# Performance work log

Hardware: AMD Instinct MI355X
Metric: run time of the kernel (lower is better)

Reference implementation:

```python
import jax, jax.numpy as jnp
import numpy as np

B, T, V, RNN, N_OBJ = 1024, 48, 2000, 64, 25

def _lstm_cell(x, h, c, W_ih, W_hh, b_ih, b_hh):
    # PyTorch LSTMCell: gate order i, f, g, o
    gates = x @ W_ih.T + h @ W_hh.T + b_ih + b_hh
    i, f, g, o = jnp.split(gates, 4, axis=-1)
    c2 = jax.nn.sigmoid(f) * c + jax.nn.sigmoid(i) * jnp.tanh(g)
    return jax.nn.sigmoid(o) * jnp.tanh(c2), c2

def _attend(memory, h2, w1, b1, w2, b2):
    # memory: [B, 25, 4], h2: [B, 25, RNN]
    x = jnp.concatenate([h2, memory], axis=2)            # [B, 25, RNN+4]
    s = (jax.nn.relu(x @ w1.T + b1) @ w2.T + b2)[..., 0]  # [B, 25]
    w = jax.nn.softmax(s, axis=1)
    return jnp.einsum('bn,bnd->bd', w, memory)            # [B, 4]

def setup_inputs() -> dict:
    key = jax.random.key(0)
    ks = jax.random.split(key, 32)
    f = lambda k, shape: jax.random.normal(k, shape, dtype=jnp.float32) * 0.05
    return dict(
        inst=jax.random.randint(ks[0], (B, T), 1, V + 1),
        prev_canvas=jax.random.uniform(ks[1], (B, N_OBJ, 4), dtype=jnp.float32),
        final_canvas=jax.random.uniform(ks[2], (B, N_OBJ, 4), dtype=jnp.float32),
        embed=f(ks[3], (V + 1, 64)),
        W_ih_att=f(ks[4], (4 * RNN, 128)), W_hh_att=f(ks[5], (4 * RNN, RNN)),
        b_ih_att=f(ks[6], (4 * RNN,)), b_hh_att=f(ks[7], (4 * RNN,)),
        W_ih_lang=f(ks[8], (4 * RNN, 2 * RNN)), W_hh_lang=f(ks[9], (4 * RNN, RNN)),
        b_ih_lang=f(ks[10], (4 * RNN,)), b_hh_lang=f(ks[11], (4 * RNN,)),
        fc_out_w=f(ks[12], (V + 1, RNN)), fc_out_b=f(ks[13], (V + 1,)),
        att1_w1=f(ks[14], (32, RNN + 4)), att1_b1=f(ks[15], (32,)),
        att1_w2=f(ks[16], (1, 32)), att1_b2=f(ks[17], (1,)),
        att2_w1=f(ks[18], (32, RNN + 4)), att2_b1=f(ks[19], (32,)),
        att2_w2=f(ks[20], (1, 32)), att2_b2=f(ks[21], (1,)),
        trans_w1=f(ks[22], (32, 8)), trans_b1=f(ks[23], (32,)),
        trans_w2=f(ks[24], (RNN, 32)), trans_b2=f(ks[25], (RNN,)),
    )

def reference(inst, prev_canvas, final_canvas, embed, W_ih_att, W_hh_att, b_ih_att, b_hh_att, W_ih_lang, W_hh_lang, b_ih_lang, b_hh_lang, fc_out_w, fc_out_b, att1_w1, att1_b1, att1_w2, att1_b2, att2_w1, att2_b1, att2_w2, att2_b2, trans_w1, trans_b1, trans_w2, trans_b2):
    # compute_diff_canvas
    mask = prev_canvas.sum(axis=2, keepdims=True) > 0
    diff_canvas = jnp.where(mask, -1.0, final_canvas)  # [B, 25, 4]
    batch = inst.shape[0]
    h0 = jnp.zeros((batch, RNN), dtype=jnp.float32)

    def step(carry, it):
        h_att, c_att, h_lang, c_lang = carry
        xt = embed[it]  # [B, 64]
        h_att, c_att = _lstm_cell(jnp.concatenate([h_lang, xt], axis=1), h_att, c_att, W_ih_att, W_hh_att, b_ih_att, b_hh_att)
        h2 = jnp.broadcast_to(h_att[:, None, :], (batch, N_OBJ, RNN))
        a1 = _attend(diff_canvas, h2, att1_w1, att1_b1, att1_w2, att1_b2)
        a2 = _attend(prev_canvas, h2, att2_w1, att2_b1, att2_w2, att2_b2)
        att = jnp.concatenate([a1, a2], axis=1)  # [B, 8]
        att = jax.nn.relu(att @ trans_w1.T + trans_b1) @ trans_w2.T + trans_b2  # [B, RNN]
        h_lang, c_lang = _lstm_cell(jnp.concatenate([att, h_att], axis=1), h_lang, c_lang, W_ih_lang, W_hh_lang, b_ih_lang, b_hh_lang)
        logp = jax.nn.log_softmax(h_lang @ fc_out_w.T + fc_out_b, axis=1)  # [B, V+1]
        return (h_att, c_att, h_lang, c_lang), logp

    xs = inst[:, :-1].T  # [T-1, B]; inst has no all-zero column so all steps run
    _, outs = jax.lax.scan(step, (h0, h0, h0, h0), xs)
    return jnp.transpose(outs, (1, 0, 2))  # [B, T-1, V+1]
```

## Files before the change

### kernel.cpp

```cpp
#include <hip/hip_runtime.h>

#define BATCH 1024
#define TT 48
#define NSTEP 47
#define VOC 2001
#define RNN 64
#define NOBJ 25
#define NROWS (BATCH*NSTEP)
#define NTILE 126
#define NPAD 2016

typedef _Float16 h2 __attribute__((ext_vector_type(2)));
typedef _Float16 h8 __attribute__((ext_vector_type(8)));
typedef short short8 __attribute__((ext_vector_type(8)));
typedef float f32x4 __attribute__((ext_vector_type(4)));

__device__ __forceinline__ float fdot2f(h2 a, h2 b, float c){
#if __has_builtin(__builtin_amdgcn_fdot2)
    return __builtin_amdgcn_fdot2(a, b, c, false);
#else
    return c + (float)a[0]*(float)b[0] + (float)a[1]*(float)b[1];
#endif
}

__device__ __forceinline__ float dot8(h8 w, h8 x, float acc){
    acc = fdot2f(__builtin_shufflevector(w,w,0,1), __builtin_shufflevector(x,x,0,1), acc);
    acc = fdot2f(__builtin_shufflevector(w,w,2,3), __builtin_shufflevector(x,x,2,3), acc);
    acc = fdot2f(__builtin_shufflevector(w,w,4,5), __builtin_shufflevector(x,x,4,5), acc);
    acc = fdot2f(__builtin_shufflevector(w,w,6,7), __builtin_shufflevector(x,x,6,7), acc);
    return acc;
}

__device__ __forceinline__ float sigf(float x){ return 1.f/(1.f+__expf(-x)); }
__device__ __forceinline__ float tanh_(float x){
    float e = __expf(2.f*fminf(x, 15.f));
    return (e-1.f)/(e+1.f);
}
__device__ __forceinline__ unsigned short bf16r(float f){
    unsigned u = __float_as_uint(f);
    return (unsigned short)((u + 0x7FFFu + ((u>>16)&1u)) >> 16);
}

__device__ __forceinline__ void block_sync_lds(){
    asm volatile("s_waitcnt lgkmcnt(0)" ::: "memory");
    __builtin_amdgcn_s_barrier();
    asm volatile("" ::: "memory");
}


__global__ void k_pre(const float* __restrict__ prev, const float* __restrict__ fin,
                      const float* __restrict__ a1w1, const float* __restrict__ a1b1,
                      const float* __restrict__ a2w1, const float* __restrict__ a2b1,
                      float* __restrict__ diff, float* __restrict__ pre1, float* __restrict__ pre2){
    int idx = blockIdx.x*256 + threadIdx.x;
    if (idx >= BATCH*NOBJ) return;
    float p0 = prev[idx*4+0], p1 = prev[idx*4+1], p2 = prev[idx*4+2], p3 = prev[idx*4+3];
    bool masked = (p0+p1+p2+p3) > 0.f;
    float d0 = masked ? -1.f : fin[idx*4+0];
    float d1 = masked ? -1.f : fin[idx*4+1];
    float d2 = masked ? -1.f : fin[idx*4+2];
    float d3 = masked ? -1.f : fin[idx*4+3];
    diff[idx*4+0]=d0; diff[idx*4+1]=d1; diff[idx*4+2]=d2; diff[idx*4+3]=d3;
    for (int j=0;j<32;++j){
        const float* w1 = a1w1 + j*68 + 64;
        const float* w2 = a2w1 + j*68 + 64;
        pre1[idx*32+j] = a1b1[j] + d0*w1[0] + d1*w1[1] + d2*w1[2] + d3*w1[3];
        pre2[idx*32+j] = a2b1[j] + p0*w2[0] + p1*w2[1] + p2*w2[2] + p3*w2[3];
    }
}

__global__ void k_embw(const float* __restrict__ embed, const float* __restrict__ Wia,
                       const float* __restrict__ bia, const float* __restrict__ bha,
                       float* __restrict__ embW){
    int v = blockIdx.x, g = threadIdx.x;
    __shared__ float er[64];
    if (g < 64) er[g] = embed[v*64+g];
    __syncthreads();
    float acc = bia[g] + bha[g];
    const float* wr = Wia + g*128 + 64;
    #pragma unroll 8
    for (int k=0;k<64;++k) acc += er[k]*wr[k];
    embW[v*256+g] = acc;
}

__global__ void k_packrow(const float* __restrict__ src, _Float16* __restrict__ dst,
                          int srcK, int koff, int K, int total){
    int idx = blockIdx.x*256 + threadIdx.x;
    if (idx >= total) return;
    int k = idx % K, g = idx / K;
    dst[idx] = (_Float16)src[g*srcK + koff + k];
}

__global__ void k_weff(const float* __restrict__ Wil, const float* __restrict__ tw2,
                       const float* __restrict__ tb2, const float* __restrict__ bil,
                       const float* __restrict__ bhl, _Float16* __restrict__ Weff,
                       float* __restrict__ biasL2){
    __shared__ float t2[64*32];
    int g = threadIdx.x;
    for (int i=g;i<2048;i+=256) t2[i] = tw2[i];
    __syncthreads();
    float accs[32];
    #pragma unroll
    for (int m=0;m<32;++m) accs[m]=0.f;
    float bf = bil[g] + bhl[g];
    for (int d=0;d<64;++d){
        float w = Wil[g*128 + d];
        bf += w * tb2[d];
        #pragma unroll
        for (int m=0;m<32;++m) accs[m] += w * t2[d*32+m];
    }
    #pragma unroll
    for (int m=0;m<32;++m) Weff[g*32+m] = (_Float16)accs[m];
    biasL2[g] = bf;
}

__global__ void k_fcbpad(const float* __restrict__ fcb_in, float* __restrict__ fcb){
    int i = blockIdx.x*256 + threadIdx.x;
    if (i >= NPAD) return;
    fcb[i] = (i < VOC) ? fcb_in[i] : -1e30f;
}

__global__ void k_fragb(const float* __restrict__ fcw, unsigned short* __restrict__ fragB){
    int idx = blockIdx.x*256 + threadIdx.x;
    int lane = idx & 63, kh = (idx>>6)&1, tile = idx>>7;
    int n = tile*16 + (lane & 15);
    int k = kh*32 + (lane >> 4)*8;
    unsigned short* d = fragB + (size_t)((tile*2+kh)*64 + lane)*8;
    #pragma unroll
    for (int i=0;i<8;++i)
        d[i] = (n < VOC) ? bf16r(fcw[n*64 + k + i]) : (unsigned short)0;
}

__global__ __launch_bounds__(256, 2) void k_recur(
    const int* __restrict__ inst, const float* __restrict__ embW,
    const float* __restrict__ diff, const float* __restrict__ prev,
    const float* __restrict__ pre1, const float* __restrict__ pre2,
    const _Float16* __restrict__ attLp, const _Float16* __restrict__ attHp,
    const _Float16* __restrict__ wLhap, const _Float16* __restrict__ wLhlp,
    const _Float16* __restrict__ Weffp, const float* __restrict__ biasL2,
    const _Float16* __restrict__ w1fp,
    const float* __restrict__ a1w2, const float* __restrict__ a1b2,
    const float* __restrict__ a2w2, const float* __restrict__ a2b2,
    const float* __restrict__ tw1, const float* __restrict__ tb1,
    unsigned short* __restrict__ h_hist)
{
    const int tid = threadIdx.x;
    const int rb0 = blockIdx.x*2;

    __shared__ float gbuf[2][256];
    __shared__ __align__(16) _Float16 hl16[2][64];
    __shared__ __align__(16) _Float16 ha16[2][64];
    __shared__ __align__(16) _Float16 u16v[2][32];
    __shared__ float hpart[2][64];
    __shared__ float sbuf[2][2][32];
    __shared__ float att8s[2][8];
    __shared__ __align__(16) float preS[2][2][25][36];
    __shared__ float memS[2][200];
    __shared__ __align__(16) _Float16 w1fS[64*72];
    __shared__ float tw1T[256];
    __shared__ float w2S[2][32];
    __shared__ float b2S[2];
    __shared__ int   tokS[2][NSTEP];

    for (int i=tid;i<2*NSTEP;i+=256){ int r=i/NSTEP, s=i-r*NSTEP; tokS[r][s]=inst[(rb0+r)*TT+s]; }
    for (int i=tid;i<3200;i+=256){
        int r = i/1600, rem = i - r*1600, h = rem/800, rem2 = rem - h*800, n = rem2>>5, k = rem2&31;
        preS[r][h][n][k] = (h ? pre2 : pre1)[(size_t)((rb0+r)*NOBJ+n)*32 + k];
    }
    for (int i=tid;i<400;i+=256){
        int r = i/200, rem = i - r*200;
        memS[r][rem] = (rem<100 ? diff : prev)[(size_t)(rb0+r)*100 + (rem%100)];
    }
    for (int i=tid;i<4096;i+=256){
        int rw = i>>6, k = i&63;
        w1fS[rw*72+k] = w1fp[i];
    }
    { int m = tid&31, k = tid>>5; tw1T[k*32+m] = tw1[m*8+k]; }
    if (tid<64) w2S[tid>>5][tid&31] = (tid<32 ? a1w2 : a2w2)[tid&31];
    if (tid<2)  b2S[tid] = tid ? a2b2[0] : a1b2[0];
    for (int i=tid;i<128;i+=256){ hl16[i>>6][i&63]=(_Float16)0.f; ha16[i>>6][i&63]=(_Float16)0.f; }

    h8 wAL[8], wAH[8], wLHa[8], wLHl[8], wEf[4];
    {
        const h8* p0 = (const h8*)(attLp + (size_t)tid*64);
        const h8* p1 = (const h8*)(attHp + (size_t)tid*64);
        const h8* p2 = (const h8*)(wLhap + (size_t)tid*64);
        const h8* p3 = (const h8*)(wLhlp + (size_t)tid*64);
        const h8* p4 = (const h8*)(Weffp + (size_t)tid*32);
        #pragma unroll
        for (int k=0;k<8;++k){ wAL[k]=p0[k]; wAH[k]=p1[k]; wLHa[k]=p2[k]; wLHl[k]=p3[k]; }
        #pragma unroll
        for (int k=0;k<4;++k) wEf[k]=p4[k];
    }
    const float biasv = biasL2[tid];
    const float tb1v  = ((tid&63) < 32) ? tb1[tid&63] : 0.f;
    float c_att = 0.f, c_lang = 0.f;
    __syncthreads();

    const int wave = tid>>6, lane = tid&63;

    const h8* xh0 = (const h8*)&hl16[0][0];
    const h8* xh1 = (const h8*)&hl16[1][0];
    const h8* xa0 = (const h8*)&ha16[0][0];
    const h8* xa1 = (const h8*)&ha16[1][0];
    const h8* xu0 = (const h8*)&u16v[0][0];
    const h8* xu1 = (const h8*)&u16v[1][0];

    float ew0 = embW[(size_t)tokS[0][0]*256 + tid];
    float ew1 = embW[(size_t)tokS[1][0]*256 + tid];

    #pragma unroll 1
    for (int t=0;t<NSTEP;++t){
        float a0 = ew0, a1 = ew1, p0 = biasv, p1 = biasv;
        {
            int tn = (t+1 < NSTEP) ? t+1 : NSTEP-1;
            ew0 = embW[(size_t)tokS[0][tn]*256 + tid];
            ew1 = embW[(size_t)tokS[1][tn]*256 + tid];
        }
        #pragma unroll
        for (int k=0;k<8;++k){
            h8 h0 = xh0[k], h1 = xh1[k];
            a0 = dot8(wAL[k],  h0, a0);  a1 = dot8(wAL[k],  h1, a1);
            p0 = dot8(wLHl[k], h0, p0);  p1 = dot8(wLHl[k], h1, p1);
        }
        #pragma unroll
        for (int k=0;k<8;++k){
            h8 v0 = xa0[k], v1 = xa1[k];
            a0 = dot8(wAH[k], v0, a0);   a1 = dot8(wAH[k], v1, a1);
        }
        gbuf[0][tid] = a0; gbuf[1][tid] = a1;
        block_sync_lds();

        if (wave < 2){
            const int r = wave;
            float gi = gbuf[r][lane], gf = gbuf[r][64+lane];
            float gg = gbuf[r][128+lane], go = gbuf[r][192+lane];
            float i_=sigf(gi), f_=sigf(gf), g_=tanh_(gg), o_=sigf(go);
            c_att = f_*c_att + i_*g_;
            ha16[r][lane] = (_Float16)(o_*tanh_(c_att));
            {
                const h8* xa = (const h8*)&ha16[r][0];
                const h8* wr = (const h8*)&w1fS[lane*72];
                float hp = 0.f;
                #pragma unroll
                for (int k=0;k<8;++k) hp = dot8(wr[k], xa[k], hp);
                hpart[r][lane] = hp;
            }
            {
                int half = lane>>5, n = lane&31;
                if (n < NOBJ){
                    const float4* pp = (const float4*)&preS[r][half][n][0];
                    const float*  hp = &hpart[r][half*32];
                    const float*  w2 = &w2S[half][0];
                    float a = b2S[half];
                    #pragma unroll
                    for (int i=0;i<8;++i){
                        float4 pv = pp[i];
                        a += fmaxf(hp[4*i+0]+pv.x,0.f)*w2[4*i+0]
                           + fmaxf(hp[4*i+1]+pv.y,0.f)*w2[4*i+1]
                           + fmaxf(hp[4*i+2]+pv.z,0.f)*w2[4*i+2]
                           + fmaxf(hp[4*i+3]+pv.w,0.f)*w2[4*i+3];
                    }
                    sbuf[r][half][n] = a;
                }
            }
            if (lane < 8){
                int half = lane>>2, d = lane&3;
                const float* ss  = &sbuf[r][half][0];
                const float* mem = &memS[r][half*100];
                float m = -1e30f;
                for (int n=0;n<NOBJ;++n) m = fmaxf(m, ss[n]);
                float s=0.f, a=0.f;
                for (int n=0;n<NOBJ;++n){ float e=__expf(ss[n]-m); s+=e; a+=e*mem[n*4+d]; }
                att8s[r][lane] = a/s;
            }
            if (lane < 32){
                float u = tb1v;
                #pragma unroll
                for (int i=0;i<8;++i) u += att8s[r][i]*tw1T[i*32+lane];
                u16v[r][lane] = (_Float16)fmaxf(u, 0.f);
            }
        }
        block_sync_lds();

        #pragma unroll
        for (int k=0;k<4;++k){
            h8 u0 = xu0[k], u1 = xu1[k];
            p0 = dot8(wEf[k], u0, p0);   p1 = dot8(wEf[k], u1, p1);
        }
        #pragma unroll
        for (int k=0;k<8;++k){
            h8 v0 = xa0[k], v1 = xa1[k];
            p0 = dot8(wLHa[k], v0, p0);  p1 = dot8(wLHa[k], v1, p1);
        }
        gbuf[0][tid] = p0; gbuf[1][tid] = p1;
        block_sync_lds();

        if (wave < 2){
            const int r = wave;
            float gi = gbuf[r][lane], gf = gbuf[r][64+lane];
            float gg = gbuf[r][128+lane], go = gbuf[r][192+lane];
            float i_=sigf(gi), f_=sigf(gf), g_=tanh_(gg), o_=sigf(go);
            c_lang = f_*c_lang + i_*g_;
            float hL = o_*tanh_(c_lang);
            hl16[r][lane] = (_Float16)hL;
            h_hist[((size_t)(rb0+r)*NSTEP + t)*64 + lane] = bf16r(hL);
        }
        block_sync_lds();
    }
}


__global__ __launch_bounds__(256) void k_fc(const unsigned short* __restrict__ h_hist,
                                            const unsigned short* __restrict__ fragB,
                                            const float* __restrict__ fcb,
                                            float* __restrict__ out)
{
    const int tid = threadIdx.x;
    const int w = tid >> 6, lane = tid & 63;
    const int q = lane >> 4, l16 = lane & 15;
    const int rowbase = blockIdx.x*16;

    const short8 a0 = *(const short8*)(h_hist + (size_t)(rowbase + l16)*64 + q*8);
    const short8 a1 = *(const short8*)(h_hist + (size_t)(rowbase + l16)*64 + 32 + q*8);

    float m[4], s[4];
    #pragma unroll
    for (int i=0;i<4;++i){ m[i] = -INFINITY; s[i] = 0.f; }

    for (int tile = w; tile < NTILE; tile += 4){
        const short8 b0 = *(const short8*)(fragB + (size_t)((tile*2+0)*64 + lane)*8);
        const short8 b1 = *(const short8*)(fragB + (size_t)((tile*2+1)*64 + lane)*8);
        f32x4 acc = {0.f,0.f,0.f,0.f};
        acc = __builtin_amdgcn_mfma_f32_16x16x32_bf16(a0, b0, acc, 0, 0, 0);
        acc = __builtin_amdgcn_mfma_f32_16x16x32_bf16(a1, b1, acc, 0, 0, 0);
        float bias = fcb[tile*16 + l16];
        #pragma unroll
        for (int i=0;i<4;++i){
            float v = acc[i] + bias;
            float nm = fmaxf(m[i], v);
            s[i] = s[i]*__expf(m[i]-nm) + __expf(v-nm);
            m[i] = nm;
        }
    }
    #pragma unroll
    for (int i=0;i<4;++i){
        #pragma unroll
        for (int off=1; off<16; off<<=1){
            float om = __shfl_xor(m[i], off, 64);
            float os = __shfl_xor(s[i], off, 64);
            float nm = fmaxf(m[i], om);
            s[i] = s[i]*__expf(m[i]-nm) + os*__expf(om-nm);
            m[i] = nm;
        }
    }
    __shared__ float lm[4][16], ls[4][16], fm[16], fl[16];
    if (l16 == 0){
        #pragma unroll
        for (int i=0;i<4;++i){ lm[w][q*4+i] = m[i]; ls[w][q*4+i] = s[i]; }
    }
    __syncthreads();
    if (tid < 16){
        float M = -INFINITY, S = 0.f;
        #pragma unroll
        for (int ww=0;ww<4;++ww){
            float om = lm[ww][tid], os = ls[ww][tid];
            float nm = fmaxf(M, om);
            S = S*__expf(M-nm) + os*__expf(om-nm);
            M = nm;
        }
        fm[tid] = M; fl[tid] = __logf(S);
    }
    __syncthreads();
    float Mr[4], Lr[4];
    #pragma unroll
    for (int i=0;i<4;++i){ Mr[i] = fm[q*4+i]; Lr[i] = fl[q*4+i]; }

    for (int tile = w; tile < NTILE; tile += 4){
        const short8 b0 = *(const short8*)(fragB + (size_t)((tile*2+0)*64 + lane)*8);
        const short8 b1 = *(const short8*)(fragB + (size_t)((tile*2+1)*64 + lane)*8);
        f32x4 acc = {0.f,0.f,0.f,0.f};
        acc = __builtin_amdgcn_mfma_f32_16x16x32_bf16(a0, b0, acc, 0, 0, 0);
        acc = __builtin_amdgcn_mfma_f32_16x16x32_bf16(a1, b1, acc, 0, 0, 0);
        int col = tile*16 + l16;
        if (col < VOC){
            float bias = fcb[col];
            #pragma unroll
            for (int i=0;i<4;++i)
                out[(size_t)(rowbase + q*4 + i)*VOC + col] = acc[i] + bias - Mr[i] - Lr[i];
        }
    }
}


extern "C" void kernel_launch(void* const* d_in, const int* in_sizes, int n_in,
                              void* d_out, int out_size, void* d_ws, size_t ws_size,
                              hipStream_t stream)
{
    const int*   inst  = (const int*)  d_in[0];
    const float* prev  = (const float*)d_in[1];
    const float* fin   = (const float*)d_in[2];
    const float* embed = (const float*)d_in[3];
    const float* Wia   = (const float*)d_in[4];
    const float* Wha   = (const float*)d_in[5];
    const float* bia   = (const float*)d_in[6];
    const float* bha   = (const float*)d_in[7];
    const float* Wil   = (const float*)d_in[8];
    const float* Whl   = (const float*)d_in[9];
    const float* bil   = (const float*)d_in[10];
    const float* bhl   = (const float*)d_in[11];
    const float* fcw   = (const float*)d_in[12];
    const float* fcbi  = (const float*)d_in[13];
    const float* a1w1  = (const float*)d_in[14];
    const float* a1b1  = (const float*)d_in[15];
    const float* a1w2  = (const float*)d_in[16];
    const float* a1b2  = (const float*)d_in[17];
    const float* a2w1  = (const float*)d_in[18];
    const float* a2b1  = (const float*)d_in[19];
    const float* a2w2  = (const float*)d_in[20];
    const float* a2b2  = (const float*)d_in[21];
    const float* tw1   = (const float*)d_in[22];
    const float* tb1   = (const float*)d_in[23];
    const float* tw2   = (const float*)d_in[24];
    const float* tb2   = (const float*)d_in[25];
    float* out = (float*)d_out;

    char* wsb = (char*)d_ws; size_t off = 0;
    auto alloc = [&](size_t bytes)->char*{
        char* p = wsb + off; off = (off + bytes + 511) & ~(size_t)511; return p;
    };
    float*          embW  = (float*)alloc((size_t)VOC*256*4);
    float*          diff  = (float*)alloc((size_t)BATCH*NOBJ*4*4);
    float*          pre1  = (float*)alloc((size_t)BATCH*NOBJ*32*4);
    float*          pre2  = (float*)alloc((size_t)BATCH*NOBJ*32*4);
    _Float16*       attLp = (_Float16*)alloc((size_t)256*64*2);
    _Float16*       attHp = (_Float16*)alloc((size_t)256*64*2);
    _Float16*       wLhap = (_Float16*)alloc((size_t)256*64*2);
    _Float16*       wLhlp = (_Float16*)alloc((size_t)256*64*2);
    _Float16*       Weffp = (_Float16*)alloc((size_t)256*32*2);
    _Float16*       w1fp  = (_Float16*)alloc((size_t)64*64*2);
    float*          biasL2= (float*)alloc(256*4);
    float*          fcb   = (float*)alloc((size_t)NPAD*4);
    unsigned short* hhist = (unsigned short*)alloc((size_t)NROWS*64*2);
    unsigned short* fragB = (unsigned short*)alloc((size_t)NTILE*2*64*8*2);

    k_pre    <<<(BATCH*NOBJ+255)/256, 256, 0, stream>>>(prev, fin, a1w1, a1b1, a2w1, a2b1, diff, pre1, pre2);
    k_embw   <<<VOC, 256, 0, stream>>>(embed, Wia, bia, bha, embW);
    k_packrow<<<64, 256, 0, stream>>>(Wia, attLp, 128, 0,  64, 256*64);
    k_packrow<<<64, 256, 0, stream>>>(Wha, attHp,  64, 0,  64, 256*64);
    k_packrow<<<64, 256, 0, stream>>>(Wil, wLhap, 128, 64, 64, 256*64);
    k_packrow<<<64, 256, 0, stream>>>(Whl, wLhlp,  64, 0,  64, 256*64);
    k_packrow<<<8,  256, 0, stream>>>(a1w1, w1fp,       68, 0, 64, 32*64);
    k_packrow<<<8,  256, 0, stream>>>(a2w1, w1fp+32*64, 68, 0, 64, 32*64);
    k_weff   <<<1, 256, 0, stream>>>(Wil, tw2, tb2, bil, bhl, Weffp, biasL2);
    k_fcbpad <<<(NPAD+255)/256, 256, 0, stream>>>(fcbi, fcb);
    k_fragb  <<<63, 256, 0, stream>>>(fcw, fragB);

    k_recur<<<BATCH/2, 256, 0, stream>>>(inst, embW, diff, prev, pre1, pre2,
                                         attLp, attHp, wLhap, wLhlp, Weffp, biasL2, w1fp,
                                         a1w2, a1b2, a2w2, a2b2, tw1, tb1, hhist);

    k_fc<<<NROWS/16, 256, 0, stream>>>(hhist, fragB, fcb, out);
}
```

Measured before the change: 828.8 us.

## Split recurrent gate dot products across two thread halves and use shuffle-based softmax

The recurrent kernel now launches 512 threads per block; each half computes half of the K dimension for every gate row, and the partial sums are added when the gates are read from LDS. This halves the per-thread weight registers and the serial dot-product chain per step, which shortens the latency-bound recurrence. The attention softmax and weighted sum are also rewritten to use wave shuffles instead of a serial 25-iteration loop over LDS in 8 lanes. The cost is more threads per block, an extra LDS read per gate, and larger register and occupancy pressure under the new launch bounds.

```diff
diff --git a/kernel.cpp b/kernel.cpp
--- a/kernel.cpp
+++ b/kernel.cpp
@@ -131,7 +131,7 @@
         d[i] = (n < VOC) ? bf16r(fcw[n*64 + k + i]) : (unsigned short)0;
 }
 
-__global__ __launch_bounds__(256, 2) void k_recur(
+__global__ __launch_bounds__(512, 4) void k_recur(
     const int* __restrict__ inst, const float* __restrict__ embW,
     const float* __restrict__ diff, const float* __restrict__ prev,
     const float* __restrict__ pre1, const float* __restrict__ pre2,
@@ -144,97 +144,102 @@
     const float* __restrict__ tw1, const float* __restrict__ tb1,
     unsigned short* __restrict__ h_hist)
 {
-    const int tid = threadIdx.x;
-    const int rb0 = blockIdx.x*2;
-
-    __shared__ float gbuf[2][256];
+    const int tid  = threadIdx.x;
+    const int g    = tid & 255;
+    const int hh   = tid >> 8;
+    const int wave = tid >> 6, lane = tid & 63;
+    const int rb0  = blockIdx.x*2;
+
+    __shared__ float pbuf[2][2][256];
     __shared__ __align__(16) _Float16 hl16[2][64];
     __shared__ __align__(16) _Float16 ha16[2][64];
     __shared__ __align__(16) _Float16 u16v[2][32];
-    __shared__ float hpart[2][64];
-    __shared__ float sbuf[2][2][32];
-    __shared__ float att8s[2][8];
+    __shared__ __align__(16) float hpart[2][64];
     __shared__ __align__(16) float preS[2][2][25][36];
-    __shared__ float memS[2][200];
+    __shared__ __align__(16) float memS[2][200];
     __shared__ __align__(16) _Float16 w1fS[64*72];
     __shared__ float tw1T[256];
-    __shared__ float w2S[2][32];
+    __shared__ __align__(16) float w2S[2][32];
     __shared__ float b2S[2];
     __shared__ int   tokS[2][NSTEP];
 
-    for (int i=tid;i<2*NSTEP;i+=256){ int r=i/NSTEP, s=i-r*NSTEP; tokS[r][s]=inst[(rb0+r)*TT+s]; }
-    for (int i=tid;i<3200;i+=256){
+    for (int i=tid;i<2*NSTEP;i+=512){ int r=i/NSTEP, s=i-r*NSTEP; tokS[r][s]=inst[(rb0+r)*TT+s]; }
+    for (int i=tid;i<3200;i+=512){
         int r = i/1600, rem = i - r*1600, h = rem/800, rem2 = rem - h*800, n = rem2>>5, k = rem2&31;
         preS[r][h][n][k] = (h ? pre2 : pre1)[(size_t)((rb0+r)*NOBJ+n)*32 + k];
     }
-    for (int i=tid;i<400;i+=256){
+    for (int i=tid;i<400;i+=512){
         int r = i/200, rem = i - r*200;
         memS[r][rem] = (rem<100 ? diff : prev)[(size_t)(rb0+r)*100 + (rem%100)];
     }
-    for (int i=tid;i<4096;i+=256){
+    for (int i=tid;i<4096;i+=512){
         int rw = i>>6, k = i&63;
         w1fS[rw*72+k] = w1fp[i];
     }
-    { int m = tid&31, k = tid>>5; tw1T[k*32+m] = tw1[m*8+k]; }
+    if (tid<256){ int m = tid&31, k = tid>>5; tw1T[k*32+m] = tw1[m*8+k]; }
     if (tid<64) w2S[tid>>5][tid&31] = (tid<32 ? a1w2 : a2w2)[tid&31];
     if (tid<2)  b2S[tid] = tid ? a2b2[0] : a1b2[0];
-    for (int i=tid;i<128;i+=256){ hl16[i>>6][i&63]=(_Float16)0.f; ha16[i>>6][i&63]=(_Float16)0.f; }
-
-    h8 wAL[8], wAH[8], wLHa[8], wLHl[8], wEf[4];
+    if (tid<128){ hl16[tid>>6][tid&63]=(_Float16)0.f; ha16[tid>>6][tid&63]=(_Float16)0.f; }
+
+    h8 wAL[4], wAH[4], wLHa[4], wLHl[4], wEf[2];
     {
-        const h8* p0 = (const h8*)(attLp + (size_t)tid*64);
-        const h8* p1 = (const h8*)(attHp + (size_t)tid*64);
-        const h8* p2 = (const h8*)(wLhap + (size_t)tid*64);
-        const h8* p3 = (const h8*)(wLhlp + (size_t)tid*64);
-        const h8* p4 = (const h8*)(Weffp + (size_t)tid*32);
-        #pragma unroll
-        for (int k=0;k<8;++k){ wAL[k]=p0[k]; wAH[k]=p1[k]; wLHa[k]=p2[k]; wLHl[k]=p3[k]; }
-        #pragma unroll
-        for (int k=0;k<4;++k) wEf[k]=p4[k];
-    }
-    const float biasv = biasL2[tid];
-    const float tb1v  = ((tid&63) < 32) ? tb1[tid&63] : 0.f;
+        const h8* p0 = (const h8*)(attLp + (size_t)g*64 + hh*32);
+        const h8* p1 = (const h8*)(attHp + (size_t)g*64 + hh*32);
+        const h8* p2 = (const h8*)(wLhap + (size_t)g*64 + hh*32);
+        const h8* p3 = (const h8*)(wLhlp + (size_t)g*64 + hh*32);
+        const h8* p4 = (const h8*)(Weffp + (size_t)g*32 + hh*16);
+        #pragma unroll
+        for (int k=0;k<4;++k){ wAL[k]=p0[k]; wAH[k]=p1[k]; wLHa[k]=p2[k]; wLHl[k]=p3[k]; }
+        wEf[0]=p4[0]; wEf[1]=p4[1];
+    }
+    const float biasv = hh ? 0.f : biasL2[g];
+    const float tb1v  = (lane < 32) ? tb1[lane] : 0.f;
     float c_att = 0.f, c_lang = 0.f;
     __syncthreads();
 
-    const int wave = tid>>6, lane = tid&63;
-
-    const h8* xh0 = (const h8*)&hl16[0][0];
-    const h8* xh1 = (const h8*)&hl16[1][0];
-    const h8* xa0 = (const h8*)&ha16[0][0];
-    const h8* xa1 = (const h8*)&ha16[1][0];
-    const h8* xu0 = (const h8*)&u16v[0][0];
-    const h8* xu1 = (const h8*)&u16v[1][0];
-
-    float ew0 = embW[(size_t)tokS[0][0]*256 + tid];
-    float ew1 = embW[(size_t)tokS[1][0]*256 + tid];
+    const h8* xh0 = (const h8*)&hl16[0][hh*32];
+    const h8* xh1 = (const h8*)&hl16[1][hh*32];
+    const h8* xa0 = (const h8*)&ha16[0][hh*32];
+    const h8* xa1 = (const h8*)&ha16[1][hh*32];
+    const h8* xu0 = (const h8*)&u16v[0][hh*16];
+    const h8* xu1 = (const h8*)&u16v[1][hh*16];
+
+    float ew0 = 0.f, ew1 = 0.f;
+    if (hh == 0){
+        ew0 = embW[(size_t)tokS[0][0]*256 + g];
+        ew1 = embW[(size_t)tokS[1][0]*256 + g];
+    }
 
     #pragma unroll 1
     for (int t=0;t<NSTEP;++t){
-        float a0 = ew0, a1 = ew1, p0 = biasv, p1 = biasv;
-        {
+        float a0 = hh ? 0.f : ew0;
+        float a1 = hh ? 0.f : ew1;
+        float p0 = biasv, p1 = biasv;
+        if (hh == 0){
             int tn = (t+1 < NSTEP) ? t+1 : NSTEP-1;
-            ew0 = embW[(size_t)tokS[0][tn]*256 + tid];
-            ew1 = embW[(size_t)tokS[1][tn]*256 + tid];
-        }
-        #pragma unroll
-        for (int k=0;k<8;++k){
+            ew0 = embW[(size_t)tokS[0][tn]*256 + g];
+            ew1 = embW[(size_t)tokS[1][tn]*256 + g];
+        }
+        #pragma unroll
+        for (int k=0;k<4;++k){
             h8 h0 = xh0[k], h1 = xh1[k];
             a0 = dot8(wAL[k],  h0, a0);  a1 = dot8(wAL[k],  h1, a1);
             p0 = dot8(wLHl[k], h0, p0);  p1 = dot8(wLHl[k], h1, p1);
         }
         #pragma unroll
-        for (int k=0;k<8;++k){
+        for (int k=0;k<4;++k){
             h8 v0 = xa0[k], v1 = xa1[k];
             a0 = dot8(wAH[k], v0, a0);   a1 = dot8(wAH[k], v1, a1);
         }
-        gbuf[0][tid] = a0; gbuf[1][tid] = a1;
+        pbuf[hh][0][g] = a0; pbuf[hh][1][g] = a1;
         block_sync_lds();
 
         if (wave < 2){
             const int r = wave;
-            float gi = gbuf[r][lane], gf = gbuf[r][64+lane];
-            float gg = gbuf[r][128+lane], go = gbuf[r][192+lane];
+            float gi = pbuf[0][r][lane]     + pbuf[1][r][lane];
+            float gf = pbuf[0][r][64+lane]  + pbuf[1][r][64+lane];
+            float gg = pbuf[0][r][128+lane] + pbuf[1][r][128+lane];
+            float go = pbuf[0][r][192+lane] + pbuf[1][r][192+lane];
             float i_=sigf(gi), f_=sigf(gf), g_=tanh_(gg), o_=sigf(go);
             c_att = f_*c_att + i_*g_;
             ha16[r][lane] = (_Float16)(o_*tanh_(c_att));
@@ -246,60 +251,71 @@
                 for (int k=0;k<8;++k) hp = dot8(wr[k], xa[k], hp);
                 hpart[r][lane] = hp;
             }
+            const int half = lane>>5, n = lane&31;
+            float sc;
             {
-                int half = lane>>5, n = lane&31;
-                if (n < NOBJ){
-                    const float4* pp = (const float4*)&preS[r][half][n][0];
-                    const float*  hp = &hpart[r][half*32];
-                    const float*  w2 = &w2S[half][0];
-                    float a = b2S[half];
-                    #pragma unroll
-                    for (int i=0;i<8;++i){
-                        float4 pv = pp[i];
-                        a += fmaxf(hp[4*i+0]+pv.x,0.f)*w2[4*i+0]
-                           + fmaxf(hp[4*i+1]+pv.y,0.f)*w2[4*i+1]
-                           + fmaxf(hp[4*i+2]+pv.z,0.f)*w2[4*i+2]
-                           + fmaxf(hp[4*i+3]+pv.w,0.f)*w2[4*i+3];
-                    }
-                    sbuf[r][half][n] = a;
+                const float4* pp  = (const float4*)&preS[r][half][(n<NOBJ)?n:0][0];
+                const float4* hp4 = (const float4*)&hpart[r][half*32];
+                const float4* wv4 = (const float4*)&w2S[half][0];
+                float a = b2S[half];
+                #pragma unroll
+                for (int i=0;i<8;++i){
+                    float4 pv = pp[i], hv = hp4[i], wv = wv4[i];
+                    a += fmaxf(hv.x+pv.x,0.f)*wv.x + fmaxf(hv.y+pv.y,0.f)*wv.y
+                       + fmaxf(hv.z+pv.z,0.f)*wv.z + fmaxf(hv.w+pv.w,0.f)*wv.w;
                 }
+                sc = (n < NOBJ) ? a : -INFINITY;
             }
-            if (lane < 8){
-                int half = lane>>2, d = lane&3;
-                const float* ss  = &sbuf[r][half][0];
-                const float* mem = &memS[r][half*100];
-                float m = -1e30f;
-                for (int n=0;n<NOBJ;++n) m = fmaxf(m, ss[n]);
-                float s=0.f, a=0.f;
-                for (int n=0;n<NOBJ;++n){ float e=__expf(ss[n]-m); s+=e; a+=e*mem[n*4+d]; }
-                att8s[r][lane] = a/s;
+            float mx = sc;
+            #pragma unroll
+            for (int off=16; off; off>>=1) mx = fmaxf(mx, __shfl_xor(mx, off, 32));
+            float e = __expf(sc - mx);
+            float4 mm = {0.f,0.f,0.f,0.f};
+            if (n < NOBJ) mm = ((const float4*)&memS[r][half*100])[n];
+            float s = e, v0 = e*mm.x, v1 = e*mm.y, v2 = e*mm.z, v3 = e*mm.w;
+            #pragma unroll
+            for (int off=16; off; off>>=1){
+                s  += __shfl_xor(s,  off, 32);
+                v0 += __shfl_xor(v0, off, 32);
+                v1 += __shfl_xor(v1, off, 32);
+                v2 += __shfl_xor(v2, off, 32);
+                v3 += __shfl_xor(v3, off, 32);
             }
+            float s1 = __shfl(s,  32|lane, 64);
+            float w0 = __shfl(v0, 32|lane, 64);
+            float w1 = __shfl(v1, 32|lane, 64);
+            float w2 = __shfl(v2, 32|lane, 64);
+            float w3 = __shfl(v3, 32|lane, 64);
             if (lane < 32){
-                float u = tb1v;
-                #pragma unroll
-                for (int i=0;i<8;++i) u += att8s[r][i]*tw1T[i*32+lane];
+                float inv0 = 1.f/s, inv1 = 1.f/s1;
+                float u = tb1v
+                    + (v0*inv0)*tw1T[0*32+lane] + (v1*inv0)*tw1T[1*32+lane]
+                    + (v2*inv0)*tw1T[2*32+lane] + (v3*inv0)*tw1T[3*32+lane]
+                    + (w0*inv1)*tw1T[4*32+lane] + (w1*inv1)*tw1T[5*32+lane]
+                    + (w2*inv1)*tw1T[6*32+lane] + (w3*inv1)*tw1T[7*32+lane];
                 u16v[r][lane] = (_Float16)fmaxf(u, 0.f);
             }
         }
         block_sync_lds();
 
         #pragma unroll
+        for (int k=0;k<2;++k){
+            p0 = dot8(wEf[k], xu0[k], p0);   p1 = dot8(wEf[k], xu1[k], p1);
+        }
+        #pragma unroll
         for (int k=0;k<4;++k){
-            h8 u0 = xu0[k], u1 = xu1[k];
-            p0 = dot8(wEf[k], u0, p0);   p1 = dot8(wEf[k], u1, p1);
-        }
-        #pragma unroll
-        for (int k=0;k<8;++k){
             h8 v0 = xa0[k], v1 = xa1[k];
             p0 = dot8(wLHa[k], v0, p0);  p1 = dot8(wLHa[k], v1, p1);
         }
-        gbuf[0][tid] = p0; gbuf[1][tid] = p1;
+        pbuf[hh][0][g] = p0; pbuf[hh][1][g] = p1;
         block_sync_lds();
 
         if (wave < 2){
             const int r = wave;
-            float gi = gbuf[r][lane], gf = gbuf[r][64+lane];
-            float gg = gbuf[r][128+lane], go = gbuf[r][192+lane];
+            float gi = pbuf[0][r][lane]     + pbuf[1][r][lane];
+            float gf = pbuf[0][r][64+lane]  + pbuf[1][r][64+lane];
+            float gg = pbuf[0][r][128+lane] + pbuf[1][r][128+lane];
+            float go = pbuf[0][r][192+lane] + pbuf[1][r][192+lane];
             float i_=sigf(gi), f_=sigf(gf), g_=tanh_(gg), o_=sigf(go);
             c_lang = f_*c_lang + i_*g_;
             float hL = o_*tanh_(c_lang);
@@ -456,7 +472,7 @@
     k_fcbpad <<<(NPAD+255)/256, 256, 0, stream>>>(fcbi, fcb);
     k_fragb  <<<63, 256, 0, stream>>>(fcw, fragB);
 
-    k_recur<<<BATCH/2, 256, 0, stream>>>(inst, embW, diff, prev, pre1, pre2,
+    k_recur<<<BATCH/2, 512, 0, stream>>>(inst, embW, diff, prev, pre1, pre2,
                                          attLp, attHp, wLhap, wLhlp, Weffp, biasL2, w1fp,
                                          a1w2, a1b2, a2w2, a2b2, tw1, tb1, hhist);
 
```

Measured after the change: 1.087 ms. 31.2% more time.
